# Kernel tuning notes

Hardware: AMD Instinct MI355X
Metric: run time of the kernel (lower is better)

Reference implementation:

```python
import jax, jax.numpy as jnp
import numpy as np

C = 512

def setup_inputs() -> dict:
    key = jax.random.key(0)
    ks = jax.random.split(key, 7)
    x = jax.random.normal(ks[0], (4, C, 64, 64), dtype=jnp.float32)
    s = 1.0 / np.sqrt(C)
    f_w = jax.random.normal(ks[1], (C // 2, C), dtype=jnp.float32) * s
    f_b = jax.random.normal(ks[2], (C // 2,), dtype=jnp.float32) * 0.01
    g_w = jax.random.normal(ks[3], (C // 2, C), dtype=jnp.float32) * s
    g_b = jax.random.normal(ks[4], (C // 2,), dtype=jnp.float32) * 0.01
    h_w = jax.random.normal(ks[5], (C, C), dtype=jnp.float32) * s
    h_b = jax.random.normal(ks[6], (C,), dtype=jnp.float32) * 0.01
    return {"x": x, "f_w": f_w, "f_b": f_b, "g_w": g_w, "g_b": g_b, "h_w": h_w, "h_b": h_b}

def reference(x, f_w, f_b, g_w, g_b, h_w, h_b):
    B, Cc, H, W = x.shape
    N = H * W
    xf = x.reshape(B, Cc, N)  # hw_flatten
    # 1x1 convs are channel GEMMs: [B,Cout,N]
    f = jnp.einsum('oc,bcn->bon', f_w, xf) + f_b[None, :, None]
    g = jnp.einsum('oc,bcn->bon', g_w, xf) + g_b[None, :, None]
    h = jnp.einsum('oc,bcn->bon', h_w, xf) + h_b[None, :, None]
    # energy[b,i,j] = sum_k f[b,k,i] * g[b,k,j]
    energy = jnp.einsum('bki,bkj->bij', f, g)
    attention = jax.nn.softmax(energy, axis=-1)
    # ret[b,c,i] = sum_j h[b,c,j] * attention[b,i,j]
    ret = jnp.einsum('bcj,bij->bci', h, attention)
    return ret.reshape(B, Cc, H, W)
```

## Files before the change

kernel.cpp:

```cpp
#include <hip/hip_runtime.h>


#define NPIX 4096
#define CIN  512

typedef _Float16 f16x4 __attribute__((ext_vector_type(4)));
typedef _Float16 f16x8 __attribute__((ext_vector_type(8)));
typedef float    f32x4 __attribute__((ext_vector_type(4)));
typedef float    f32x16 __attribute__((ext_vector_type(16)));

#define MFMA16(a, b, c) __builtin_amdgcn_mfma_f32_16x16x16f16(a, b, c, 0, 0, 0)
#define MFMA32(a, b, c) __builtin_amdgcn_mfma_f32_32x32x16_f16(a, b, c, 0, 0, 0)

__device__ __forceinline__ void gld_lds16(const void* g, void* l) {
    __builtin_amdgcn_global_load_lds(
        (const __attribute__((address_space(1))) unsigned int*)g,
        (__attribute__((address_space(3))) unsigned int*)l, 16, 0, 0);
}

__global__ __launch_bounds__(256) void proj_kernel(
    const float* __restrict__ x,
    const float* __restrict__ f_w, const float* __restrict__ f_b,
    const float* __restrict__ g_w, const float* __restrict__ g_b,
    const float* __restrict__ h_w, const float* __restrict__ h_b,
    _Float16* __restrict__ qw, _Float16* __restrict__ kw,
    _Float16* __restrict__ vw)
{
    const int b  = blockIdx.z;
    const int n0 = blockIdx.x * 64;
    const int o0 = blockIdx.y * 64;

    const float* wsrc; const float* bsrc;
    if (o0 < 256)      { wsrc = f_w + (size_t)o0 * CIN;         bsrc = f_b + o0; }
    else if (o0 < 512) { wsrc = g_w + (size_t)(o0 - 256) * CIN; bsrc = g_b + (o0 - 256); }
    else               { wsrc = h_w + (size_t)(o0 - 512) * CIN; bsrc = h_b + (o0 - 512); }

    __shared__ _Float16 Wt[64][40];
    __shared__ _Float16 Xt[64][40];

    const int t = threadIdx.x;
    const int lane = t & 63, wv = t >> 6;
    const int wm = wv >> 1, wn = wv & 1;
    const int gi = lane >> 4, li = lane & 15;

    f32x4 acc[2][2];
    #pragma unroll
    for (int i = 0; i < 2; ++i)
        #pragma unroll
        for (int j = 0; j < 2; ++j) acc[i][j] = f32x4{0.f, 0.f, 0.f, 0.f};

    for (int kk = 0; kk < CIN; kk += 32) {
        {
            const int r = t >> 2, c8 = (t & 3) * 8;
            const float* p = wsrc + (size_t)r * CIN + kk + c8;
            const float4 v0 = *(const float4*)p;
            const float4 v1 = *(const float4*)(p + 4);
            f16x8 w8;
            w8[0] = (_Float16)v0.x; w8[1] = (_Float16)v0.y;
            w8[2] = (_Float16)v0.z; w8[3] = (_Float16)v0.w;
            w8[4] = (_Float16)v1.x; w8[5] = (_Float16)v1.y;
            w8[6] = (_Float16)v1.z; w8[7] = (_Float16)v1.w;
            *(f16x8*)&Wt[r][c8] = w8;
        }
        {
            const int cb = (t >> 6) * 8;
            const int nl = t & 63;
            f16x8 xv;
            #pragma unroll
            for (int e = 0; e < 8; ++e)
                xv[e] = (_Float16)x[((size_t)b * CIN + kk + cb + e) * NPIX +
                                    n0 + nl];
            *(f16x8*)&Xt[nl][cb] = xv;
        }
        __syncthreads();
        #pragma unroll
        for (int kh = 0; kh < 2; ++kh) {
            const int ko = kh * 16 + gi * 4;
            f16x4 a0 = *(const f16x4*)&Wt[wm * 32 +      li][ko];
            f16x4 a1 = *(const f16x4*)&Wt[wm * 32 + 16 + li][ko];
            f16x4 b0 = *(const f16x4*)&Xt[wn * 32 +      li][ko];
            f16x4 b1 = *(const f16x4*)&Xt[wn * 32 + 16 + li][ko];
            acc[0][0] = MFMA16(a0, b0, acc[0][0]);
            acc[0][1] = MFMA16(a0, b1, acc[0][1]);
            acc[1][0] = MFMA16(a1, b0, acc[1][0]);
            acc[1][1] = MFMA16(a1, b1, acc[1][1]);
        }
        __syncthreads();
    }

    #pragma unroll
    for (int mf = 0; mf < 2; ++mf)
        #pragma unroll
        for (int nf = 0; nf < 2; ++nf) {
            const int obase = o0 + wm * 32 + mf * 16 + gi * 4;
            const int n     = n0 + wn * 32 + nf * 16 + li;
            const int brel  = wm * 32 + mf * 16 + gi * 4;
            float v[4];
            #pragma unroll
            for (int r = 0; r < 4; ++r) v[r] = acc[mf][nf][r] + bsrc[brel + r];
            if (o0 < 512) {
                _Float16* dst = (o0 < 256) ? qw : kw;
                const int kb  = (o0 < 256) ? obase : (obase - 256);
                f16x4 pk;
                pk[0] = (_Float16)v[0]; pk[1] = (_Float16)v[1];
                pk[2] = (_Float16)v[2]; pk[3] = (_Float16)v[3];
                *(f16x4*)&dst[((size_t)b * NPIX + n) * 256 + kb] = pk;
            } else {
                #pragma unroll
                for (int r = 0; r < 4; ++r)
                    vw[((size_t)b * CIN + (obase - 512 + r)) * NPIX + n] =
                        (_Float16)v[r];
            }
        }
}

__global__ __launch_bounds__(512, 2) void attn_kernel(
    const _Float16* __restrict__ qw, const _Float16* __restrict__ kw,
    const _Float16* __restrict__ vw,
    _Float16* __restrict__ opart, float* __restrict__ stats)
{
    const int bid = blockIdx.x;
    const int xcd = bid & 7;
    const int jh = xcd & 1, b = xcd >> 1;
    const int rb = bid >> 3;
    const int t = threadIdx.x, l = t & 63, wv = t >> 6;
    const int li = l & 31, g = l >> 5;
    const int ch = wv >> 2, rg = wv & 3;
    const int tc = t & 255;
    const int i_row = rb * 128 + rg * 32 + li;

    __shared__ char Kt[2][16384];
    __shared__ char Vt[2][512 * 72];
    __shared__ char Pt[2][4][64 * 48];

    f16x8 qf[16];
    if (ch == 0) {
        const _Float16* qb = qw + ((size_t)b * NPIX + i_row) * 256 + 8 * g;
        #pragma unroll
        for (int ks = 0; ks < 16; ++ks) qf[ks] = *(const f16x8*)(qb + ks * 16);
    }

    f32x16 oacc[8];
    #pragma unroll
    for (int i = 0; i < 8; ++i)
        #pragma unroll
        for (int e = 0; e < 16; ++e) oacc[i][e] = 0.f;
    float m_run = -__builtin_inff();
    float l_run = 0.f;

    f16x8 vreg[4];

    auto stageK = [&](int buf, int j0) {
        #pragma unroll
        for (int q = 0; q < 4; ++q) {
            const int slot = q * 256 + tc;
            const int row  = slot >> 5;
            const int colb = (slot & 31) * 16;
            const char* src =
                (const char*)(kw + ((size_t)b * NPIX + j0 + row) * 256) +
                (colb ^ ((row & 31) << 4));
            gld_lds16(src, Kt[buf] + slot * 16);
        }
    };
    auto loadVh = [&](int half, int j0) {
        #pragma unroll
        for (int q = 0; q < 4; ++q) {
            const int c = half * 256 + q * 64 + (tc >> 2);
            vreg[q] = *(const f16x8*)(vw + ((size_t)b * CIN + c) * NPIX + j0 +
                                      (tc & 3) * 8);
        }
    };
    auto writeVh = [&](int buf, int half) {
        #pragma unroll
        for (int q = 0; q < 4; ++q) {
            const int c = half * 256 + q * 64 + (tc >> 2);
            char* d = Vt[buf] + c * 72 + (tc & 3) * 16;
            *(f16x4*)d       = *(f16x4*)&vreg[q];
            *(f16x4*)(d + 8) = *((f16x4*)&vreg[q] + 1);
        }
    };

    const int jbase = jh * 2048;
    if (ch == 0) {
        stageK(0, jbase);
    } else {
        loadVh(0, jbase); writeVh(0, 0);
        loadVh(1, jbase); writeVh(0, 1);
    }
    __syncthreads();

    for (int s = 0; s < 64; ++s) {
        const int cur = s & 1;
        f16x8 pa0, pa1;

        if (ch == 0) {
            if (s < 63) stageK(cur ^ 1, jbase + (s + 1) * 32);

            f32x16 sv;
            #pragma unroll
            for (int e = 0; e < 16; ++e) sv[e] = 0.f;
            {
                const char* kr = Kt[cur] + li * 512;
                const int sw = li << 4;
                __builtin_amdgcn_s_setprio(1);
                #pragma unroll
                for (int ks = 0; ks < 16; ++ks) {
                    f16x8 kf = *(const f16x8*)(kr + ((ks * 32 + 16 * g) ^ sw));
                    sv = MFMA32(kf, qf[ks], sv);
                }
                __builtin_amdgcn_s_setprio(0);
            }

            float tmax = sv[0];
            #pragma unroll
            for (int e = 1; e < 16; ++e) tmax = fmaxf(tmax, sv[e]);
            tmax = fmaxf(tmax, __shfl_xor(tmax, 32));
            float sc_my = 1.0f;
            if (!__all((int)(tmax - m_run <= 5.f))) {
                const float mnew = fmaxf(m_run, tmax);
                sc_my = __expf(m_run - mnew);
                #pragma unroll
                for (int ct = 0; ct < 8; ++ct)
                    #pragma unroll
                    for (int e = 0; e < 16; ++e) oacc[ct][e] *= sc_my;
                l_run *= sc_my;
                m_run = mnew;
            }
            float p[16];
            float rs = 0.f;
            #pragma unroll
            for (int e = 0; e < 16; ++e) { p[e] = __expf(sv[e] - m_run); rs += p[e]; }
            rs += __shfl_xor(rs, 32);
            l_run += rs;

            #pragma unroll
            for (int e = 0; e < 8; ++e) {
                pa0[e] = (_Float16)p[e];
                pa1[e] = (_Float16)p[8 + e];
            }
            char* pd = Pt[cur][rg] + l * 48;
            *(f16x8*)pd        = pa0;
            *(f16x8*)(pd + 16) = pa1;
            *(float*)(pd + 32) = sc_my;
        } else {
            if (s < 63) loadVh(0, jbase + (s + 1) * 32);
        }

        __syncthreads();

        if (ch == 0) {
            __builtin_amdgcn_s_setprio(1);
            #pragma unroll
            for (int ct = 0; ct < 8; ++ct) {
                const int c = ct * 32 + li;
                const char* vr = Vt[cur] + c * 72;
                f16x8 va, vc;
                *(f16x4*)&va       = *(const f16x4*)(vr + 8 * g);
                *((f16x4*)&va + 1) = *(const f16x4*)(vr + 16 + 8 * g);
                oacc[ct] = MFMA32(va, pa0, oacc[ct]);
                *(f16x4*)&vc       = *(const f16x4*)(vr + 32 + 8 * g);
                *((f16x4*)&vc + 1) = *(const f16x4*)(vr + 48 + 8 * g);
                oacc[ct] = MFMA32(vc, pa1, oacc[ct]);
            }
            __builtin_amdgcn_s_setprio(0);
        } else {
            if (s < 63) {
                writeVh(cur ^ 1, 0);
                loadVh(1, jbase + (s + 1) * 32);
            }
            const char* ps = Pt[cur][rg] + l * 48;
            pa0 = *(const f16x8*)ps;
            pa1 = *(const f16x8*)(ps + 16);
            const float sc = *(const float*)(ps + 32);
            if (!__all((int)(sc == 1.0f))) {
                #pragma unroll
                for (int ct = 0; ct < 8; ++ct)
                    #pragma unroll
                    for (int e = 0; e < 16; ++e) oacc[ct][e] *= sc;
            }
            __builtin_amdgcn_s_setprio(1);
            #pragma unroll
            for (int ct = 0; ct < 8; ++ct) {
                const int c = 256 + ct * 32 + li;
                const char* vr = Vt[cur] + c * 72;
                f16x8 va, vc;
                *(f16x4*)&va       = *(const f16x4*)(vr + 8 * g);
                *((f16x4*)&va + 1) = *(const f16x4*)(vr + 16 + 8 * g);
                oacc[ct] = MFMA32(va, pa0, oacc[ct]);
                *(f16x4*)&vc       = *(const f16x4*)(vr + 32 + 8 * g);
                *((f16x4*)&vc + 1) = *(const f16x4*)(vr + 48 + 8 * g);
                oacc[ct] = MFMA32(vc, pa1, oacc[ct]);
            }
            __builtin_amdgcn_s_setprio(0);
            if (s < 63) writeVh(cur ^ 1, 1);
        }
    }

    const size_t ob = (size_t)(jh * 4 + b) * CIN * NPIX;
    #pragma unroll
    for (int ct = 0; ct < 8; ++ct)
        #pragma unroll
        for (int r = 0; r < 16; ++r) {
            const int c = ch * 256 + ct * 32 + (r & 3) + 8 * (r >> 2) + 4 * g;
            opart[ob + (size_t)c * NPIX + i_row] = (_Float16)oacc[ct][r];
        }
    if (ch == 0 && g == 0) {
        const size_t idx = ((size_t)(jh * 4 + b) * NPIX + i_row) * 2;
        stats[idx]     = m_run;
        stats[idx + 1] = l_run;
    }
}

__global__ __launch_bounds__(256) void combine_kernel(
    const _Float16* __restrict__ opart, const float* __restrict__ stats,
    float* __restrict__ out)
{
    const int b  = blockIdx.y;
    const int i0 = blockIdx.x * 64;
    const int t  = threadIdx.x;

    __shared__ float a0s[64], a1s[64];
    if (t < 64) {
        const int i = i0 + t;
        const size_t r0 = ((size_t)b * NPIX + i) * 2;
        const size_t r1 = ((size_t)(4 + b) * NPIX + i) * 2;
        const float m0 = stats[r0], l0 = stats[r0 + 1];
        const float m1 = stats[r1], l1 = stats[r1 + 1];
        const float M  = fmaxf(m0, m1);
        const float w0 = __expf(m0 - M), w1 = __expf(m1 - M);
        const float inv = 1.0f / (l0 * w0 + l1 * w1);
        a0s[t] = w0 * inv;
        a1s[t] = w1 * inv;
    }
    __syncthreads();

    const int ci = t >> 3;
    const int ii = (t & 7) * 8;
    #pragma unroll 4
    for (int pp = 0; pp < 16; ++pp) {
        const int c = pp * 32 + ci;
        const _Float16* p0 = opart + ((size_t)b * CIN + c) * NPIX + i0 + ii;
        const _Float16* p1 = opart + ((size_t)(4 + b) * CIN + c) * NPIX + i0 + ii;
        const f16x8 x0 = *(const f16x8*)p0;
        const f16x8 x1 = *(const f16x8*)p1;
        float* dst = out + ((size_t)b * CIN + c) * NPIX + i0 + ii;
        float4 o0, o1;
        o0.x = a0s[ii + 0] * (float)x0[0] + a1s[ii + 0] * (float)x1[0];
        o0.y = a0s[ii + 1] * (float)x0[1] + a1s[ii + 1] * (float)x1[1];
        o0.z = a0s[ii + 2] * (float)x0[2] + a1s[ii + 2] * (float)x1[2];
        o0.w = a0s[ii + 3] * (float)x0[3] + a1s[ii + 3] * (float)x1[3];
        o1.x = a0s[ii + 4] * (float)x0[4] + a1s[ii + 4] * (float)x1[4];
        o1.y = a0s[ii + 5] * (float)x0[5] + a1s[ii + 5] * (float)x1[5];
        o1.z = a0s[ii + 6] * (float)x0[6] + a1s[ii + 6] * (float)x1[6];
        o1.w = a0s[ii + 7] * (float)x0[7] + a1s[ii + 7] * (float)x1[7];
        *(float4*)dst       = o0;
        *(float4*)(dst + 4) = o1;
    }
}

extern "C" void kernel_launch(void* const* d_in, const int* in_sizes, int n_in,
                              void* d_out, int out_size, void* d_ws,
                              size_t ws_size, hipStream_t stream)
{
    const float* x   = (const float*)d_in[0];
    const float* f_w = (const float*)d_in[1];
    const float* f_b = (const float*)d_in[2];
    const float* g_w = (const float*)d_in[3];
    const float* g_b = (const float*)d_in[4];
    const float* h_w = (const float*)d_in[5];
    const float* h_b = (const float*)d_in[6];
    float* out = (float*)d_out;

    _Float16* qw = (_Float16*)d_ws;
    _Float16* kw = qw + (size_t)4 * NPIX * 256;
    _Float16* vw = kw + (size_t)4 * NPIX * 256;
    _Float16* op = vw + (size_t)4 * CIN * NPIX;
    float* stats = (float*)(op + (size_t)2 * 4 * CIN * NPIX);

    proj_kernel<<<dim3(64, 16, 4), 256, 0, stream>>>(
        x, f_w, f_b, g_w, g_b, h_w, h_b, qw, kw, vw);
    attn_kernel<<<dim3(256), 512, 0, stream>>>(qw, kw, vw, op, stats);
    combine_kernel<<<dim3(64, 4), 256, 0, stream>>>(op, stats, out);
}
```

Before: 236.8 us.

## Fold log2e into query projection and double-buffer projection LDS tiles

The query projection weights and bias are pre-scaled by log2(e), so the attention and combine kernels can use exp2 directly instead of __expf, which multiplies by log2e internally. This saves a multiply per exponential in the softmax inner loop, and the lazy-rescale threshold is adjusted to the equivalent base-2 value. The projection kernel also gains double-buffered LDS tiles, so the next K-slice is staged while MFMAs run on the current one, removing one barrier per iteration. Scaling the query weights before fp16 conversion slightly changes rounding.

```diff
diff --git a/kernel.cpp b/kernel.cpp
--- a/kernel.cpp
+++ b/kernel.cpp
@@ -3,6 +3,7 @@
 
 #define NPIX 4096
 #define CIN  512
+#define LOG2E 1.44269504f
 
 typedef _Float16 f16x4 __attribute__((ext_vector_type(4)));
 typedef _Float16 f16x8 __attribute__((ext_vector_type(8)));
@@ -30,13 +31,13 @@
     const int n0 = blockIdx.x * 64;
     const int o0 = blockIdx.y * 64;
 
-    const float* wsrc; const float* bsrc;
-    if (o0 < 256)      { wsrc = f_w + (size_t)o0 * CIN;         bsrc = f_b + o0; }
-    else if (o0 < 512) { wsrc = g_w + (size_t)(o0 - 256) * CIN; bsrc = g_b + (o0 - 256); }
-    else               { wsrc = h_w + (size_t)(o0 - 512) * CIN; bsrc = h_b + (o0 - 512); }
-
-    __shared__ _Float16 Wt[64][40];
-    __shared__ _Float16 Xt[64][40];
+    const float* wsrc; const float* bsrc; float wscale;
+    if (o0 < 256)      { wsrc = f_w + (size_t)o0 * CIN;         bsrc = f_b + o0;         wscale = LOG2E; }
+    else if (o0 < 512) { wsrc = g_w + (size_t)(o0 - 256) * CIN; bsrc = g_b + (o0 - 256); wscale = 1.0f; }
+    else               { wsrc = h_w + (size_t)(o0 - 512) * CIN; bsrc = h_b + (o0 - 512); wscale = 1.0f; }
+
+    __shared__ _Float16 Wt[2][64][40];
+    __shared__ _Float16 Xt[2][64][40];
 
     const int t = threadIdx.x;
     const int lane = t & 63, wv = t >> 6;
@@ -49,18 +50,18 @@
         #pragma unroll
         for (int j = 0; j < 2; ++j) acc[i][j] = f32x4{0.f, 0.f, 0.f, 0.f};
 
-    for (int kk = 0; kk < CIN; kk += 32) {
+    auto stage = [&](int buf, int kk) {
         {
             const int r = t >> 2, c8 = (t & 3) * 8;
             const float* p = wsrc + (size_t)r * CIN + kk + c8;
             const float4 v0 = *(const float4*)p;
             const float4 v1 = *(const float4*)(p + 4);
             f16x8 w8;
-            w8[0] = (_Float16)v0.x; w8[1] = (_Float16)v0.y;
-            w8[2] = (_Float16)v0.z; w8[3] = (_Float16)v0.w;
-            w8[4] = (_Float16)v1.x; w8[5] = (_Float16)v1.y;
-            w8[6] = (_Float16)v1.z; w8[7] = (_Float16)v1.w;
-            *(f16x8*)&Wt[r][c8] = w8;
+            w8[0] = (_Float16)(v0.x * wscale); w8[1] = (_Float16)(v0.y * wscale);
+            w8[2] = (_Float16)(v0.z * wscale); w8[3] = (_Float16)(v0.w * wscale);
+            w8[4] = (_Float16)(v1.x * wscale); w8[5] = (_Float16)(v1.y * wscale);
+            w8[6] = (_Float16)(v1.z * wscale); w8[7] = (_Float16)(v1.w * wscale);
+            *(f16x8*)&Wt[buf][r][c8] = w8;
         }
         {
             const int cb = (t >> 6) * 8;
@@ -70,16 +71,23 @@
             for (int e = 0; e < 8; ++e)
                 xv[e] = (_Float16)x[((size_t)b * CIN + kk + cb + e) * NPIX +
                                     n0 + nl];
-            *(f16x8*)&Xt[nl][cb] = xv;
-        }
-        __syncthreads();
+            *(f16x8*)&Xt[buf][nl][cb] = xv;
+        }
+    };
+
+    stage(0, 0);
+    __syncthreads();
+
+    for (int kk = 0; kk < CIN; kk += 32) {
+        const int buf = (kk >> 5) & 1;
+        if (kk + 32 < CIN) stage(buf ^ 1, kk + 32);
         #pragma unroll
         for (int kh = 0; kh < 2; ++kh) {
             const int ko = kh * 16 + gi * 4;
-            f16x4 a0 = *(const f16x4*)&Wt[wm * 32 +      li][ko];
-            f16x4 a1 = *(const f16x4*)&Wt[wm * 32 + 16 + li][ko];
-            f16x4 b0 = *(const f16x4*)&Xt[wn * 32 +      li][ko];
-            f16x4 b1 = *(const f16x4*)&Xt[wn * 32 + 16 + li][ko];
+            f16x4 a0 = *(const f16x4*)&Wt[buf][wm * 32 +      li][ko];
+            f16x4 a1 = *(const f16x4*)&Wt[buf][wm * 32 + 16 + li][ko];
+            f16x4 b0 = *(const f16x4*)&Xt[buf][wn * 32 +      li][ko];
+            f16x4 b1 = *(const f16x4*)&Xt[buf][wn * 32 + 16 + li][ko];
             acc[0][0] = MFMA16(a0, b0, acc[0][0]);
             acc[0][1] = MFMA16(a0, b1, acc[0][1]);
             acc[1][0] = MFMA16(a1, b0, acc[1][0]);
@@ -88,6 +96,7 @@
         __syncthreads();
     }
 
+    const float bscale = wscale;
     #pragma unroll
     for (int mf = 0; mf < 2; ++mf)
         #pragma unroll
@@ -97,7 +106,8 @@
             const int brel  = wm * 32 + mf * 16 + gi * 4;
             float v[4];
             #pragma unroll
-            for (int r = 0; r < 4; ++r) v[r] = acc[mf][nf][r] + bsrc[brel + r];
+            for (int r = 0; r < 4; ++r)
+                v[r] = acc[mf][nf][r] + bsrc[brel + r] * bscale;
             if (o0 < 512) {
                 _Float16* dst = (o0 < 256) ? qw : kw;
                 const int kb  = (o0 < 256) ? obase : (obase - 256);
@@ -216,9 +226,9 @@
             for (int e = 1; e < 16; ++e) tmax = fmaxf(tmax, sv[e]);
             tmax = fmaxf(tmax, __shfl_xor(tmax, 32));
             float sc_my = 1.0f;
-            if (!__all((int)(tmax - m_run <= 5.f))) {
+            if (!__all((int)(tmax - m_run <= 7.2f))) {
                 const float mnew = fmaxf(m_run, tmax);
-                sc_my = __expf(m_run - mnew);
+                sc_my = exp2f(m_run - mnew);
                 #pragma unroll
                 for (int ct = 0; ct < 8; ++ct)
                     #pragma unroll
@@ -229,7 +239,7 @@
             float p[16];
             float rs = 0.f;
             #pragma unroll
-            for (int e = 0; e < 16; ++e) { p[e] = __expf(sv[e] - m_run); rs += p[e]; }
+            for (int e = 0; e < 16; ++e) { p[e] = exp2f(sv[e] - m_run); rs += p[e]; }
             rs += __shfl_xor(rs, 32);
             l_run += rs;
 
@@ -327,7 +337,7 @@
         const float m0 = stats[r0], l0 = stats[r0 + 1];
         const float m1 = stats[r1], l1 = stats[r1 + 1];
         const float M  = fmaxf(m0, m1);
-        const float w0 = __expf(m0 - M), w1 = __expf(m1 - M);
+        const float w0 = exp2f(m0 - M), w1 = exp2f(m1 - M);
         const float inv = 1.0f / (l0 * w0 + l1 * w1);
         a0s[t] = w0 * inv;
         a1s[t] = w1 * inv;
```

Measured after the change: 250.4 us. 5.7% more time.

## Double-buffer projection tiles and split QK MFMA chain into two accumulators

Applied to the files above, without the earlier changes.

The projection GEMM now double-buffers its W/X shared-memory tiles, so the next K-slice is staged while MFMAs run on the current one. In the attention loop, the QK^T dot product is split into two independent MFMA accumulator chains to break the serial dependency, and the row max uses a tree reduction. The rescale of the output accumulator moves after the barrier and is skipped when no lane changed its max. This costs extra LDS and registers and may lower occupancy.

```diff
diff --git a/kernel.cpp b/kernel.cpp
--- a/kernel.cpp
+++ b/kernel.cpp
@@ -35,8 +35,8 @@
     else if (o0 < 512) { wsrc = g_w + (size_t)(o0 - 256) * CIN; bsrc = g_b + (o0 - 256); }
     else               { wsrc = h_w + (size_t)(o0 - 512) * CIN; bsrc = h_b + (o0 - 512); }
 
-    __shared__ _Float16 Wt[64][40];
-    __shared__ _Float16 Xt[64][40];
+    __shared__ _Float16 Wt[2][64][40];
+    __shared__ _Float16 Xt[2][64][40];
 
     const int t = threadIdx.x;
     const int lane = t & 63, wv = t >> 6;
@@ -49,7 +49,7 @@
         #pragma unroll
         for (int j = 0; j < 2; ++j) acc[i][j] = f32x4{0.f, 0.f, 0.f, 0.f};
 
-    for (int kk = 0; kk < CIN; kk += 32) {
+    auto stage = [&](int buf, int kk) {
         {
             const int r = t >> 2, c8 = (t & 3) * 8;
             const float* p = wsrc + (size_t)r * CIN + kk + c8;
@@ -60,7 +60,7 @@
             w8[2] = (_Float16)v0.z; w8[3] = (_Float16)v0.w;
             w8[4] = (_Float16)v1.x; w8[5] = (_Float16)v1.y;
             w8[6] = (_Float16)v1.z; w8[7] = (_Float16)v1.w;
-            *(f16x8*)&Wt[r][c8] = w8;
+            *(f16x8*)&Wt[buf][r][c8] = w8;
         }
         {
             const int cb = (t >> 6) * 8;
@@ -70,16 +70,23 @@
             for (int e = 0; e < 8; ++e)
                 xv[e] = (_Float16)x[((size_t)b * CIN + kk + cb + e) * NPIX +
                                     n0 + nl];
-            *(f16x8*)&Xt[nl][cb] = xv;
-        }
-        __syncthreads();
+            *(f16x8*)&Xt[buf][nl][cb] = xv;
+        }
+    };
+
+    stage(0, 0);
+    __syncthreads();
+
+    for (int kk = 0; kk < CIN; kk += 32) {
+        const int buf = (kk >> 5) & 1;
+        if (kk + 32 < CIN) stage(buf ^ 1, kk + 32);
         #pragma unroll
         for (int kh = 0; kh < 2; ++kh) {
             const int ko = kh * 16 + gi * 4;
-            f16x4 a0 = *(const f16x4*)&Wt[wm * 32 +      li][ko];
-            f16x4 a1 = *(const f16x4*)&Wt[wm * 32 + 16 + li][ko];
-            f16x4 b0 = *(const f16x4*)&Xt[wn * 32 +      li][ko];
-            f16x4 b1 = *(const f16x4*)&Xt[wn * 32 + 16 + li][ko];
+            f16x4 a0 = *(const f16x4*)&Wt[buf][wm * 32 +      li][ko];
+            f16x4 a1 = *(const f16x4*)&Wt[buf][wm * 32 + 16 + li][ko];
+            f16x4 b0 = *(const f16x4*)&Xt[buf][wn * 32 +      li][ko];
+            f16x4 b1 = *(const f16x4*)&Xt[buf][wn * 32 + 16 + li][ko];
             acc[0][0] = MFMA16(a0, b0, acc[0][0]);
             acc[0][1] = MFMA16(a0, b1, acc[0][1]);
             acc[1][0] = MFMA16(a1, b0, acc[1][0]);
@@ -192,38 +199,43 @@
     for (int s = 0; s < 64; ++s) {
         const int cur = s & 1;
         f16x8 pa0, pa1;
+        float sc_my = 1.0f;
 
         if (ch == 0) {
             if (s < 63) stageK(cur ^ 1, jbase + (s + 1) * 32);
 
-            f32x16 sv;
-            #pragma unroll
-            for (int e = 0; e < 16; ++e) sv[e] = 0.f;
+            f32x16 sa, sb;
+            #pragma unroll
+            for (int e = 0; e < 16; ++e) { sa[e] = 0.f; sb[e] = 0.f; }
             {
                 const char* kr = Kt[cur] + li * 512;
                 const int sw = li << 4;
                 __builtin_amdgcn_s_setprio(1);
                 #pragma unroll
-                for (int ks = 0; ks < 16; ++ks) {
-                    f16x8 kf = *(const f16x8*)(kr + ((ks * 32 + 16 * g) ^ sw));
-                    sv = MFMA32(kf, qf[ks], sv);
+                for (int ks = 0; ks < 8; ++ks) {
+                    f16x8 k0 = *(const f16x8*)(kr + ((ks * 32 + 16 * g) ^ sw));
+                    f16x8 k1 = *(const f16x8*)(kr + (((ks + 8) * 32 + 16 * g) ^ sw));
+                    sa = MFMA32(k0, qf[ks], sa);
+                    sb = MFMA32(k1, qf[ks + 8], sb);
                 }
                 __builtin_amdgcn_s_setprio(0);
             }
-
-            float tmax = sv[0];
-            #pragma unroll
-            for (int e = 1; e < 16; ++e) tmax = fmaxf(tmax, sv[e]);
+            f32x16 sv;
+            #pragma unroll
+            for (int e = 0; e < 16; ++e) sv[e] = sa[e] + sb[e];
+
+            float a0 = fmaxf(fmaxf(sv[0],  sv[1]),  sv[2]);
+            float a1 = fmaxf(fmaxf(sv[3],  sv[4]),  sv[5]);
+            float a2 = fmaxf(fmaxf(sv[6],  sv[7]),  sv[8]);
+            float a3 = fmaxf(fmaxf(sv[9],  sv[10]), sv[11]);
+            float a4 = fmaxf(fmaxf(sv[12], sv[13]), sv[14]);
+            float tmax = fmaxf(fmaxf(fmaxf(a0, a1), fmaxf(a2, a3)),
+                               fmaxf(a4, sv[15]));
             tmax = fmaxf(tmax, __shfl_xor(tmax, 32));
-            float sc_my = 1.0f;
+
             if (!__all((int)(tmax - m_run <= 5.f))) {
                 const float mnew = fmaxf(m_run, tmax);
                 sc_my = __expf(m_run - mnew);
-                #pragma unroll
-                for (int ct = 0; ct < 8; ++ct)
-                    #pragma unroll
-                    for (int e = 0; e < 16; ++e) oacc[ct][e] *= sc_my;
-                l_run *= sc_my;
                 m_run = mnew;
             }
             float p[16];
@@ -231,7 +243,7 @@
             #pragma unroll
             for (int e = 0; e < 16; ++e) { p[e] = __expf(sv[e] - m_run); rs += p[e]; }
             rs += __shfl_xor(rs, 32);
-            l_run += rs;
+            l_run = l_run * sc_my + rs;
 
             #pragma unroll
             for (int e = 0; e < 8; ++e) {
@@ -249,6 +261,12 @@
         __syncthreads();
 
         if (ch == 0) {
+            if (!__all((int)(sc_my == 1.0f))) {
+                #pragma unroll
+                for (int ct = 0; ct < 8; ++ct)
+                    #pragma unroll
+                    for (int e = 0; e < 16; ++e) oacc[ct][e] *= sc_my;
+            }
             __builtin_amdgcn_s_setprio(1);
             #pragma unroll
             for (int ct = 0; ct < 8; ++ct) {
```

Result: slower. 287.4 us (+21.3%).

## Read V directly from global in attention; double-buffer projection GEMM tiles

Applied to the files above, without the earlier changes.

The attention kernel stops staging V through shared memory. Each wave now loads its V fragments straight from global memory (L2/L1) inside the PV MFMA loop, which removes the V LDS buffer and the load/write staging done by the ch==1 waves. The projection kernel gains double-buffered W and X tiles in LDS so the next k-slice is staged while the current one is multiplied. The risk is that global-load latency now sits on the MFMA critical path with no prefetch. Both channel halves also reread V from cache separately.

```diff
diff --git a/kernel.cpp b/kernel.cpp
--- a/kernel.cpp
+++ b/kernel.cpp
@@ -35,8 +35,8 @@
     else if (o0 < 512) { wsrc = g_w + (size_t)(o0 - 256) * CIN; bsrc = g_b + (o0 - 256); }
     else               { wsrc = h_w + (size_t)(o0 - 512) * CIN; bsrc = h_b + (o0 - 512); }
 
-    __shared__ _Float16 Wt[64][40];
-    __shared__ _Float16 Xt[64][40];
+    __shared__ _Float16 Wt[2][64][40];
+    __shared__ _Float16 Xt[2][64][40];
 
     const int t = threadIdx.x;
     const int lane = t & 63, wv = t >> 6;
@@ -49,7 +49,7 @@
         #pragma unroll
         for (int j = 0; j < 2; ++j) acc[i][j] = f32x4{0.f, 0.f, 0.f, 0.f};
 
-    for (int kk = 0; kk < CIN; kk += 32) {
+    auto stage = [&](int buf, int kk) {
         {
             const int r = t >> 2, c8 = (t & 3) * 8;
             const float* p = wsrc + (size_t)r * CIN + kk + c8;
@@ -60,7 +60,7 @@
             w8[2] = (_Float16)v0.z; w8[3] = (_Float16)v0.w;
             w8[4] = (_Float16)v1.x; w8[5] = (_Float16)v1.y;
             w8[6] = (_Float16)v1.z; w8[7] = (_Float16)v1.w;
-            *(f16x8*)&Wt[r][c8] = w8;
+            *(f16x8*)&Wt[buf][r][c8] = w8;
         }
         {
             const int cb = (t >> 6) * 8;
@@ -70,16 +70,23 @@
             for (int e = 0; e < 8; ++e)
                 xv[e] = (_Float16)x[((size_t)b * CIN + kk + cb + e) * NPIX +
                                     n0 + nl];
-            *(f16x8*)&Xt[nl][cb] = xv;
-        }
-        __syncthreads();
+            *(f16x8*)&Xt[buf][nl][cb] = xv;
+        }
+    };
+
+    stage(0, 0);
+    __syncthreads();
+
+    for (int kk = 0; kk < CIN; kk += 32) {
+        const int buf = (kk >> 5) & 1;
+        if (kk + 32 < CIN) stage(buf ^ 1, kk + 32);
         #pragma unroll
         for (int kh = 0; kh < 2; ++kh) {
             const int ko = kh * 16 + gi * 4;
-            f16x4 a0 = *(const f16x4*)&Wt[wm * 32 +      li][ko];
-            f16x4 a1 = *(const f16x4*)&Wt[wm * 32 + 16 + li][ko];
-            f16x4 b0 = *(const f16x4*)&Xt[wn * 32 +      li][ko];
-            f16x4 b1 = *(const f16x4*)&Xt[wn * 32 + 16 + li][ko];
+            f16x4 a0 = *(const f16x4*)&Wt[buf][wm * 32 +      li][ko];
+            f16x4 a1 = *(const f16x4*)&Wt[buf][wm * 32 + 16 + li][ko];
+            f16x4 b0 = *(const f16x4*)&Xt[buf][wn * 32 +      li][ko];
+            f16x4 b1 = *(const f16x4*)&Xt[buf][wn * 32 + 16 + li][ko];
             acc[0][0] = MFMA16(a0, b0, acc[0][0]);
             acc[0][1] = MFMA16(a0, b1, acc[0][1]);
             acc[1][0] = MFMA16(a1, b0, acc[1][0]);
@@ -130,7 +137,6 @@
     const int i_row = rb * 128 + rg * 32 + li;
 
     __shared__ char Kt[2][16384];
-    __shared__ char Vt[2][512 * 72];
     __shared__ char Pt[2][4][64 * 48];
 
     f16x8 qf[16];
@@ -147,8 +153,6 @@
         for (int e = 0; e < 16; ++e) oacc[i][e] = 0.f;
     float m_run = -__builtin_inff();
     float l_run = 0.f;
-
-    f16x8 vreg[4];
 
     auto stageK = [&](int buf, int j0) {
         #pragma unroll
@@ -162,39 +166,22 @@
             gld_lds16(src, Kt[buf] + slot * 16);
         }
     };
-    auto loadVh = [&](int half, int j0) {
-        #pragma unroll
-        for (int q = 0; q < 4; ++q) {
-            const int c = half * 256 + q * 64 + (tc >> 2);
-            vreg[q] = *(const f16x8*)(vw + ((size_t)b * CIN + c) * NPIX + j0 +
-                                      (tc & 3) * 8);
-        }
-    };
-    auto writeVh = [&](int buf, int half) {
-        #pragma unroll
-        for (int q = 0; q < 4; ++q) {
-            const int c = half * 256 + q * 64 + (tc >> 2);
-            char* d = Vt[buf] + c * 72 + (tc & 3) * 16;
-            *(f16x4*)d       = *(f16x4*)&vreg[q];
-            *(f16x4*)(d + 8) = *((f16x4*)&vreg[q] + 1);
-        }
-    };
+
+    const char* vbase =
+        (const char*)(vw + ((size_t)b * CIN + ch * 256 + li) * NPIX) + 8 * g;
 
     const int jbase = jh * 2048;
-    if (ch == 0) {
-        stageK(0, jbase);
-    } else {
-        loadVh(0, jbase); writeVh(0, 0);
-        loadVh(1, jbase); writeVh(0, 1);
-    }
+    if (ch == 0) stageK(0, jbase);
     __syncthreads();
 
     for (int s = 0; s < 64; ++s) {
         const int cur = s & 1;
+        const int j0 = jbase + s * 32;
         f16x8 pa0, pa1;
+        float sc_my = 1.0f;
 
         if (ch == 0) {
-            if (s < 63) stageK(cur ^ 1, jbase + (s + 1) * 32);
+            if (s < 63) stageK(cur ^ 1, j0 + 32);
 
             f32x16 sv;
             #pragma unroll
@@ -215,7 +202,6 @@
             #pragma unroll
             for (int e = 1; e < 16; ++e) tmax = fmaxf(tmax, sv[e]);
             tmax = fmaxf(tmax, __shfl_xor(tmax, 32));
-            float sc_my = 1.0f;
             if (!__all((int)(tmax - m_run <= 5.f))) {
                 const float mnew = fmaxf(m_run, tmax);
                 sc_my = __expf(m_run - mnew);
@@ -242,32 +228,11 @@
             *(f16x8*)pd        = pa0;
             *(f16x8*)(pd + 16) = pa1;
             *(float*)(pd + 32) = sc_my;
-        } else {
-            if (s < 63) loadVh(0, jbase + (s + 1) * 32);
         }
 
         __syncthreads();
 
-        if (ch == 0) {
-            __builtin_amdgcn_s_setprio(1);
-            #pragma unroll
-            for (int ct = 0; ct < 8; ++ct) {
-                const int c = ct * 32 + li;
-                const char* vr = Vt[cur] + c * 72;
-                f16x8 va, vc;
-                *(f16x4*)&va       = *(const f16x4*)(vr + 8 * g);
-                *((f16x4*)&va + 1) = *(const f16x4*)(vr + 16 + 8 * g);
-                oacc[ct] = MFMA32(va, pa0, oacc[ct]);
-                *(f16x4*)&vc       = *(const f16x4*)(vr + 32 + 8 * g);
-                *((f16x4*)&vc + 1) = *(const f16x4*)(vr + 48 + 8 * g);
-                oacc[ct] = MFMA32(vc, pa1, oacc[ct]);
-            }
-            __builtin_amdgcn_s_setprio(0);
-        } else {
-            if (s < 63) {
-                writeVh(cur ^ 1, 0);
-                loadVh(1, jbase + (s + 1) * 32);
-            }
+        if (ch == 1) {
             const char* ps = Pt[cur][rg] + l * 48;
             pa0 = *(const f16x8*)ps;
             pa1 = *(const f16x8*)(ps + 16);
@@ -278,21 +243,23 @@
                     #pragma unroll
                     for (int e = 0; e < 16; ++e) oacc[ct][e] *= sc;
             }
+        }
+
+        {
+            const char* vr = vbase + (size_t)j0 * 2;
             __builtin_amdgcn_s_setprio(1);
             #pragma unroll
             for (int ct = 0; ct < 8; ++ct) {
-                const int c = 256 + ct * 32 + li;
-                const char* vr = Vt[cur] + c * 72;
+                const char* vp = vr + (size_t)ct * 32 * NPIX * 2;
                 f16x8 va, vc;
-                *(f16x4*)&va       = *(const f16x4*)(vr + 8 * g);
-                *((f16x4*)&va + 1) = *(const f16x4*)(vr + 16 + 8 * g);
+                *(f16x4*)&va       = *(const f16x4*)(vp);
+                *((f16x4*)&va + 1) = *(const f16x4*)(vp + 16);
                 oacc[ct] = MFMA32(va, pa0, oacc[ct]);
-                *(f16x4*)&vc       = *(const f16x4*)(vr + 32 + 8 * g);
-                *((f16x4*)&vc + 1) = *(const f16x4*)(vr + 48 + 8 * g);
+                *(f16x4*)&vc       = *(const f16x4*)(vp + 32);
+                *((f16x4*)&vc + 1) = *(const f16x4*)(vp + 48);
                 oacc[ct] = MFMA32(vc, pa1, oacc[ct]);
             }
             __builtin_amdgcn_s_setprio(0);
-            if (s < 63) writeVh(cur ^ 1, 1);
         }
     }
 
```

Measured after the change: 605.6 us. 156% more time.
